# Kernel optimization log

Hardware: AMD Instinct MI355X
Metric: run time of the kernel (lower is better)

## Reference

```python
import jax, jax.numpy as jnp
import numpy as np

B, T, C, H = 8, 1024, 768, 12
M = 8  # extra rows in feats left as zeros (n = M + B*T)
N = M + B * T


def setup_inputs() -> dict:
    key = jax.random.key(0)
    k1, k2, k3, k4, k5 = jax.random.split(key, 5)
    feats = jax.random.normal(k1, (N, C), dtype=jnp.float32)
    amask = jax.random.randint(k2, (B, T), 0, 2).astype(bool)
    Wqkv = jax.random.normal(k3, (3 * C, C), dtype=jnp.float32) * 0.02
    Wp = jax.random.normal(k4, (C, C), dtype=jnp.float32) * 0.02
    bp = jax.random.normal(k5, (C,), dtype=jnp.float32) * 0.001
    return {"feats": feats, "amask": amask, "Wqkv": Wqkv, "Wp": Wp, "bp": bp}


def reference(feats, amask, Wqkv, Wp, bp):
    b, t = amask.shape
    n, c = feats.shape
    m = n - b * t          # rows of feats not touched by attention (stay zero)
    h = H
    d = c // h
    scale = d ** -0.5
    mf = amask.reshape(-1)                      # [b*t] bool
    x = feats[m:]                               # [b*t, c]

    # MaskedLinear(qkv): gather->GEMM->scatter == dense GEMM zeroed at masked-out rows
    qkv = jnp.where(mf[:, None], x @ Wqkv.T, jnp.zeros((), x.dtype))  # [b*t, 3c]
    qkv = qkv.reshape(b, t, 3, h, d).transpose(2, 0, 3, 1, 4)          # [3,b,h,t,d]
    q, k, v = qkv[0], qkv[1], qkv[2]

    # dense SDPA (no attn mask, matching F.scaled_dot_product_attention default)
    att = jax.nn.softmax(jnp.einsum('bhqd,bhkd->bhqk', q, k) * scale, axis=-1)
    o = jnp.einsum('bhqk,bhkd->bhqd', att, v)                          # [b,h,t,d]
    o = o.transpose(0, 2, 1, 3).reshape(b * t, c)                      # [b*t, c]

    # MaskedLinear(proj) with bias; masked-out rows are zero (not bias)
    o = jnp.where(mf[:, None], o @ Wp.T + bp, jnp.zeros((), o.dtype))

    # scatter back into a zero tensor of feats' shape (first m rows zero)
    return jnp.concatenate([jnp.zeros((m, c), feats.dtype), o], axis=0)
```

## Files before the change

### kernel.cpp

```cpp
#include <hip/hip_runtime.h>
#include <hip/hip_bf16.h>


#define BB 8
#define TT 1024
#define CC 768
#define HH 12
#define DD 64
#define MM 8
#define NTOK (BB*TT)
#define NX (NTOK*CC)
#define NWQ (3*CC*CC)
#define NWP (CC*CC)
#define QSCALE 0.18033688011112042f

typedef short bf16x4 __attribute__((ext_vector_type(4)));
typedef short bf16x8 __attribute__((ext_vector_type(8)));
typedef float f32x4  __attribute__((ext_vector_type(4)));
typedef float f32x16 __attribute__((ext_vector_type(16)));
typedef unsigned int u32x2 __attribute__((ext_vector_type(2)));

__device__ __forceinline__ void gld16(const void* g, void* l) {
  __builtin_amdgcn_global_load_lds(
      (const __attribute__((address_space(1))) void*)g,
      (__attribute__((address_space(3))) void*)l, 16, 0, 0);
}

__device__ __forceinline__ short bf_rne(float f) {
  unsigned u = __float_as_uint(f);
  return (short)((u + 0x7FFFu + ((u >> 16) & 1u)) >> 16);
}
__device__ __forceinline__ short bf_split(float f, short& lo) {
  unsigned u = __float_as_uint(f);
  unsigned hb = (u + 0x7FFFu + ((u >> 16) & 1u)) >> 16;
  float r = f - __uint_as_float(hb << 16);
  lo = bf_rne(r);
  return (short)hb;
}

__global__ __launch_bounds__(256) void split_inputs(
    const float* __restrict__ x, const float* __restrict__ wq,
    const float* __restrict__ wp,
    short* __restrict__ xh, short* __restrict__ wqh,
    short* __restrict__ wph, short* __restrict__ wpl,
    float* __restrict__ out) {
  const int G0 = NX/4, G1 = G0 + NWQ/4, G2 = G1 + NWP/4;
  int i = blockIdx.x * 256 + threadIdx.x;
  if (i < MM*CC/4) {
    float4 z = {0.f, 0.f, 0.f, 0.f};
    ((float4*)out)[i] = z;
  }
  if (i >= G2) return;
  if (i < G1) {
    const float* src = (i < G0) ? x : wq;
    short* dh = (i < G0) ? xh : wqh;
    int li = (i < G0) ? i : i - G0;
    float4 v = *(const float4*)(src + (size_t)li * 4);
    short4 h;
    h.x = bf_rne(v.x); h.y = bf_rne(v.y); h.z = bf_rne(v.z); h.w = bf_rne(v.w);
    *(short4*)(dh + (size_t)li * 4) = h;
  } else {
    int li = i - G1;
    float4 v = *(const float4*)(wp + (size_t)li * 4);
    short4 h, l;
    h.x = bf_split(v.x, l.x);
    h.y = bf_split(v.y, l.y);
    h.z = bf_split(v.z, l.z);
    h.w = bf_split(v.w, l.w);
    *(short4*)(wph + (size_t)li * 4) = h;
    *(short4*)(wpl + (size_t)li * 4) = l;
  }
}

template<bool TRIPLE>
__device__ __forceinline__ void gemm_core_768(
    const short* __restrict__ ah_g, const short* __restrict__ al_g,
    const short* __restrict__ bh_g, const short* __restrict__ bl_g,
    short* Ah, short* Al, short* Bh, short* Bl,
    int m0, int n0, f32x16 (&acc)[2][2],
    int& wm_o, int& wn_o) {
  const int tid = threadIdx.x;
  const int w = tid >> 6, ln = tid & 63;
  const int wm = (w >> 1) * 64, wn = (w & 1) * 64;
  const int sr = ln >> 2;
  const int sc = (((ln & 3) ^ ((ln >> 3) & 3))) * 8;
  const int l31 = ln & 31, lhi = ln >> 5;
  const int key = (l31 >> 1) & 3;
  const int c0 = 2*w, c1 = 2*w + 1;
  const short* gAh0 = ah_g + (size_t)(m0 + c0*16 + sr)*CC + sc;
  const short* gAh1 = ah_g + (size_t)(m0 + c1*16 + sr)*CC + sc;
  const short* gBh0 = bh_g + (size_t)(n0 + c0*16 + sr)*CC + sc;
  const short* gBh1 = bh_g + (size_t)(n0 + c1*16 + sr)*CC + sc;
  const short* gAl0 = TRIPLE ? al_g + (size_t)(m0 + c0*16 + sr)*CC + sc : nullptr;
  const short* gAl1 = TRIPLE ? al_g + (size_t)(m0 + c1*16 + sr)*CC + sc : nullptr;
  const short* gBl0 = TRIPLE ? bl_g + (size_t)(n0 + c0*16 + sr)*CC + sc : nullptr;
  const short* gBl1 = TRIPLE ? bl_g + (size_t)(n0 + c1*16 + sr)*CC + sc : nullptr;
  #pragma unroll
  for (int i = 0; i < 2; i++)
    #pragma unroll
    for (int j = 0; j < 2; j++)
      #pragma unroll
      for (int r = 0; r < 16; r++) acc[i][j][r] = 0.f;

  for (int it = 0; it < 24; ++it) {
    const int ko = it * 32;
    gld16(gAh0 + ko, &Ah[c0*512]);
    gld16(gAh1 + ko, &Ah[c1*512]);
    gld16(gBh0 + ko, &Bh[c0*512]);
    gld16(gBh1 + ko, &Bh[c1*512]);
    if constexpr (TRIPLE) {
      gld16(gAl0 + ko, &Al[c0*512]);
      gld16(gAl1 + ko, &Al[c1*512]);
      gld16(gBl0 + ko, &Bl[c0*512]);
      gld16(gBl1 + ko, &Bl[c1*512]);
    }
    __syncthreads();
    bf16x8 a_h[2][2], b_h[2][2];
    #pragma unroll
    for (int t = 0; t < 2; ++t)
      #pragma unroll
      for (int kc = 0; kc < 2; ++kc) {
        const int sA = ((kc*2 + lhi) ^ key) * 8;
        a_h[t][kc] = *(const bf16x8*)&Ah[(wm + t*32 + l31)*32 + sA];
        b_h[t][kc] = *(const bf16x8*)&Bh[(wn + t*32 + l31)*32 + sA];
      }
    if constexpr (TRIPLE) {
      bf16x8 a_l[2][2], b_l[2][2];
      #pragma unroll
      for (int t = 0; t < 2; ++t)
        #pragma unroll
        for (int kc = 0; kc < 2; ++kc) {
          const int sA = ((kc*2 + lhi) ^ key) * 8;
          a_l[t][kc] = *(const bf16x8*)&Al[(wm + t*32 + l31)*32 + sA];
          b_l[t][kc] = *(const bf16x8*)&Bl[(wn + t*32 + l31)*32 + sA];
        }
      #pragma unroll
      for (int mt = 0; mt < 2; ++mt)
        #pragma unroll
        for (int nt = 0; nt < 2; ++nt)
          #pragma unroll
          for (int kc = 0; kc < 2; ++kc) {
            acc[mt][nt] = __builtin_amdgcn_mfma_f32_32x32x16_bf16(
                a_h[mt][kc], b_h[nt][kc], acc[mt][nt], 0, 0, 0);
            acc[mt][nt] = __builtin_amdgcn_mfma_f32_32x32x16_bf16(
                a_h[mt][kc], b_l[nt][kc], acc[mt][nt], 0, 0, 0);
            acc[mt][nt] = __builtin_amdgcn_mfma_f32_32x32x16_bf16(
                a_l[mt][kc], b_h[nt][kc], acc[mt][nt], 0, 0, 0);
          }
    } else {
      #pragma unroll
      for (int mt = 0; mt < 2; ++mt)
        #pragma unroll
        for (int nt = 0; nt < 2; ++nt)
          #pragma unroll
          for (int kc = 0; kc < 2; ++kc)
            acc[mt][nt] = __builtin_amdgcn_mfma_f32_32x32x16_bf16(
                a_h[mt][kc], b_h[nt][kc], acc[mt][nt], 0, 0, 0);
    }
    __syncthreads();
  }
  wm_o = wm; wn_o = wn;
}

__global__ __launch_bounds__(256) void qkv_mfma(
    const short* __restrict__ xh, const short* __restrict__ wqh,
    const int* __restrict__ mask,
    short* __restrict__ qb, short* __restrict__ kb, short* __restrict__ vbt) {
  __shared__ __align__(16) short Ah[128*32], Bh[128*32];
  const int m0 = blockIdx.x * 128, n0 = blockIdx.y * 128;
  const int s = n0 / CC;
  f32x16 acc[2][2];
  int wm, wn;
  const int ln = threadIdx.x & 63;
  const int l31 = ln & 31, lhi = ln >> 5;

  if (s < 2) {
    gemm_core_768<false>(xh, nullptr, wqh, nullptr,
                         Ah, nullptr, Bh, nullptr, m0, n0, acc, wm, wn);
    short* dst = (s == 0) ? qb : kb;
    const float qs = (s == 0) ? QSCALE : 1.f;
    const int nb = n0 % CC;
    #pragma unroll
    for (int mt = 0; mt < 2; ++mt) {
      #pragma unroll
      for (int reg = 0; reg < 16; ++reg) {
        int row = m0 + wm + mt*32 + 4*lhi + (reg & 3) + 8*(reg >> 2);
        int mk = mask[row];
        int b = row >> 10, t = row & 1023;
        size_t rb = ((size_t)b * HH) * TT;
        #pragma unroll
        for (int nt = 0; nt < 2; ++nt) {
          int gnb = nb + wn + nt*32 + l31;
          int h = gnb >> 6, d = gnb & 63;
          float v = mk ? acc[mt][nt][reg] * qs : 0.f;
          dst[((rb + (size_t)h * TT) + t) * DD + d] = bf_rne(v);
        }
      }
    }
  } else {
    gemm_core_768<false>(wqh, nullptr, xh, nullptr,
                         Ah, nullptr, Bh, nullptr, n0, m0, acc, wm, wn);
    const int b = m0 >> 10, t0 = m0 & 1023;
    #pragma unroll
    for (int mt = 0; mt < 2; ++mt) {
      #pragma unroll
      for (int reg = 0; reg < 16; ++reg) {
        int f = (n0 - 2*CC) + wm + mt*32 + 4*lhi + (reg & 3) + 8*(reg >> 2);
        int h = f >> 6, d = f & 63;
        short* drow = vbt + (((size_t)(b*HH + h)*DD) + d)*TT + t0;
        #pragma unroll
        for (int nt = 0; nt < 2; ++nt) {
          int tk = wn + nt*32 + l31;
          int mk = mask[m0 + tk];
          drow[tk] = bf_rne(mk ? acc[mt][nt][reg] : 0.f);
        }
      }
    }
  }
}

__global__ __launch_bounds__(256) void proj_mfma(
    const short* __restrict__ ah_g, const short* __restrict__ al_g,
    const short* __restrict__ bh_g, const short* __restrict__ bl_g,
    const int* __restrict__ mask, const float* __restrict__ bp,
    float* __restrict__ out) {
  __shared__ __align__(16) short Ah[128*32], Al[128*32];
  __shared__ __align__(16) short Bh[128*32], Bl[128*32];
  const int m0 = blockIdx.x * 128, n0 = blockIdx.y * 128;
  f32x16 acc[2][2];
  int wm, wn;
  gemm_core_768<true>(ah_g, al_g, bh_g, bl_g, Ah, Al, Bh, Bl, m0, n0, acc, wm, wn);
  const int ln = threadIdx.x & 63;
  const int l31 = ln & 31, lhi = ln >> 5;
  #pragma unroll
  for (int mt = 0; mt < 2; ++mt) {
    #pragma unroll
    for (int reg = 0; reg < 16; ++reg) {
      int row = m0 + wm + mt*32 + 4*lhi + (reg & 3) + 8*(reg >> 2);
      int mk = mask[row];
      float* orow = out + (size_t)(MM + row) * CC;
      #pragma unroll
      for (int nt = 0; nt < 2; ++nt) {
        int gn = n0 + wn + nt*32 + l31;
        orow[gn] = mk ? acc[mt][nt][reg] + bp[gn] : 0.f;
      }
    }
  }
}

__device__ __forceinline__ bf16x4 tr64(unsigned addr, int imm) {
  bf16x4 r;
  asm volatile("ds_read_b64_tr_b16 %0, %1 offset:%c2"
               : "=v"(r) : "v"(addr), "i"(imm));
  return r;
}

__global__ __launch_bounds__(256, 3) void attn_mfma(
    const short* __restrict__ qb, const short* __restrict__ kb,
    const short* __restrict__ vbt, const int* __restrict__ mask,
    short* __restrict__ obh, short* __restrict__ obl) {
  __shared__ __align__(16) short Ks[64][72];
  __shared__ __align__(16) short Vt[64][72];
  __shared__ __align__(16) short PsT[4][2][64][16];
  const int tid = threadIdx.x, w = tid >> 6, ln = tid & 63;
  const int fl = ln & 15, fq = ln >> 4;
  const int i = blockIdx.x;
  const int bh = i % 96;
  const int q0 = (i / 96) * 128;
  const int b = bh / HH, h = bh % HH;
  const size_t baseK = (size_t)bh * TT * DD;
  const size_t baseV = (size_t)bh * DD * TT;

  bf16x8 qf[2][2];
  #pragma unroll
  for (int mt = 0; mt < 2; ++mt)
    #pragma unroll
    for (int kc = 0; kc < 2; ++kc)
      qf[mt][kc] = *(const bf16x8*)&qb[baseK +
          (size_t)(q0 + w*32 + mt*16 + fl) * DD + kc*32 + fq*8];

  f32x4 oa[2][4];
  float lsum[2][4];
  {
    f32x4 z = {0.f, 0.f, 0.f, 0.f};
    #pragma unroll
    for (int mt = 0; mt < 2; ++mt) {
      #pragma unroll
      for (int nt = 0; nt < 4; ++nt) oa[mt][nt] = z;
      #pragma unroll
      for (int r = 0; r < 4; ++r) lsum[mt][r] = 0.f;
    }
  }

  const unsigned ps_rd =
      (unsigned)(size_t)(&PsT[0][0][0][0]) + w*4096 + fq*256 + fl*8;

  const int srow = tid >> 2, scol = (tid & 3) * 16;
  const short* kg = &kb[baseK + (size_t)srow * DD + scol];
  const short* vg = &vbt[baseV + (size_t)srow * TT + scol];

  bf16x8 rk0 = *(const bf16x8*)kg;
  bf16x8 rk1 = *(const bf16x8*)(kg + 8);
  bf16x8 rv0 = *(const bf16x8*)vg;
  bf16x8 rv1 = *(const bf16x8*)(vg + 8);
  *(bf16x8*)&Ks[srow][scol]     = rk0;
  *(bf16x8*)&Ks[srow][scol + 8] = rk1;
  *(bf16x8*)&Vt[srow][scol]     = rv0;
  *(bf16x8*)&Vt[srow][scol + 8] = rv1;
  asm volatile("s_waitcnt lgkmcnt(0)" ::: "memory");
  __builtin_amdgcn_s_barrier();

  for (int kt = 0; kt < 16; ++kt) {
    if (kt < 15) {
      const short* kgn = kg + (size_t)(kt + 1) * 64 * DD;
      const short* vgn = vg + (kt + 1) * 64;
      rk0 = *(const bf16x8*)kgn;
      rk1 = *(const bf16x8*)(kgn + 8);
      rv0 = *(const bf16x8*)vgn;
      rv1 = *(const bf16x8*)(vgn + 8);
    }

    bf16x8 kf[4][2];
    #pragma unroll
    for (int nt = 0; nt < 4; ++nt)
      #pragma unroll
      for (int kc = 0; kc < 2; ++kc)
        kf[nt][kc] = *(const bf16x8*)&Ks[nt*16 + fl][kc*32 + fq*8];

    f32x4 s[2][4];
    {
      f32x4 z = {0.f, 0.f, 0.f, 0.f};
      #pragma unroll
      for (int mt = 0; mt < 2; ++mt)
        #pragma unroll
        for (int nt = 0; nt < 4; ++nt) s[mt][nt] = z;
    }
    #pragma unroll
    for (int mt = 0; mt < 2; ++mt)
      #pragma unroll
      for (int nt = 0; nt < 4; ++nt) {
        s[mt][nt] = __builtin_amdgcn_mfma_f32_16x16x32_bf16(
            qf[mt][0], kf[nt][0], s[mt][nt], 0, 0, 0);
        s[mt][nt] = __builtin_amdgcn_mfma_f32_16x16x32_bf16(
            qf[mt][1], kf[nt][1], s[mt][nt], 0, 0, 0);
      }

    bf16x8 vf[4][2];
    #pragma unroll
    for (int nt = 0; nt < 4; ++nt)
      #pragma unroll
      for (int kc = 0; kc < 2; ++kc)
        vf[nt][kc] = *(const bf16x8*)&Vt[nt*16 + fl][kc*32 + fq*8];

    #pragma unroll
    for (int mt = 0; mt < 2; ++mt)
      #pragma unroll
      for (int nt = 0; nt < 4; ++nt) {
        unsigned u0 = __float_as_uint(__builtin_amdgcn_exp2f(s[mt][nt][0]));
        unsigned u1 = __float_as_uint(__builtin_amdgcn_exp2f(s[mt][nt][1]));
        unsigned u2 = __float_as_uint(__builtin_amdgcn_exp2f(s[mt][nt][2]));
        unsigned u3 = __float_as_uint(__builtin_amdgcn_exp2f(s[mt][nt][3]));
        lsum[mt][0] += __uint_as_float(u0 & 0xFFFF0000u);
        lsum[mt][1] += __uint_as_float(u1 & 0xFFFF0000u);
        lsum[mt][2] += __uint_as_float(u2 & 0xFFFF0000u);
        lsum[mt][3] += __uint_as_float(u3 & 0xFFFF0000u);
        u32x2 pw;
        pw[0] = (u0 >> 16) | (u1 & 0xFFFF0000u);
        pw[1] = (u2 >> 16) | (u3 & 0xFFFF0000u);
        *(u32x2*)&PsT[w][mt][nt*16 + fl][fq*4] = pw;
      }

    asm volatile("s_waitcnt lgkmcnt(0)" ::: "memory");

    bf16x8 pf[2][2];
    #pragma unroll
    for (int mt = 0; mt < 2; ++mt)
      #pragma unroll
      for (int kc = 0; kc < 2; ++kc) {
        bf16x4 lo = tr64(ps_rd, mt*2048 + kc*1024);
        bf16x4 hi = tr64(ps_rd, mt*2048 + kc*1024 + 128);
        pf[mt][kc] = __builtin_shufflevector(lo, hi, 0, 1, 2, 3, 4, 5, 6, 7);
      }
    asm volatile("s_waitcnt lgkmcnt(0)" ::: "memory");
    __builtin_amdgcn_sched_barrier(0);

    #pragma unroll
    for (int mt = 0; mt < 2; ++mt)
      #pragma unroll
      for (int nt = 0; nt < 4; ++nt) {
        oa[mt][nt] = __builtin_amdgcn_mfma_f32_16x16x32_bf16(
            pf[mt][0], vf[nt][0], oa[mt][nt], 0, 0, 0);
        oa[mt][nt] = __builtin_amdgcn_mfma_f32_16x16x32_bf16(
            pf[mt][1], vf[nt][1], oa[mt][nt], 0, 0, 0);
      }

    __builtin_amdgcn_s_barrier();
    __builtin_amdgcn_sched_barrier(0);
    if (kt < 15) {
      *(bf16x8*)&Ks[srow][scol]     = rk0;
      *(bf16x8*)&Ks[srow][scol + 8] = rk1;
      *(bf16x8*)&Vt[srow][scol]     = rv0;
      *(bf16x8*)&Vt[srow][scol + 8] = rv1;
      asm volatile("s_waitcnt lgkmcnt(0)" ::: "memory");
    }
    __builtin_amdgcn_s_barrier();
  }

  #pragma unroll
  for (int mt = 0; mt < 2; ++mt)
    #pragma unroll
    for (int r = 0; r < 4; ++r) {
      float v = lsum[mt][r];
      v += __shfl_xor(v, 1);
      v += __shfl_xor(v, 2);
      v += __shfl_xor(v, 4);
      v += __shfl_xor(v, 8);
      lsum[mt][r] = v;
    }

  #pragma unroll
  for (int mt = 0; mt < 2; ++mt)
    #pragma unroll
    for (int r = 0; r < 4; ++r) {
      int tok = b * TT + q0 + w*32 + mt*16 + fq*4 + r;
      int mk = mask[tok];
      float inv = 1.f / lsum[mt][r];
      size_t ro = (size_t)tok * CC + h * DD;
      #pragma unroll
      for (int nt = 0; nt < 4; ++nt) {
        float v = mk ? oa[mt][nt][r] * inv : 0.f;
        short lo, hi = bf_split(v, lo);
        obh[ro + nt*16 + fl] = hi;
        obl[ro + nt*16 + fl] = lo;
      }
    }
}

extern "C" void kernel_launch(void* const* d_in, const int* in_sizes, int n_in,
                              void* d_out, int out_size, void* d_ws, size_t ws_size,
                              hipStream_t stream) {
  const float* feats = (const float*)d_in[0];
  const int*   mask  = (const int*)d_in[1];
  const float* Wqkv  = (const float*)d_in[2];
  const float* Wp    = (const float*)d_in[3];
  const float* bp    = (const float*)d_in[4];
  float* out = (float*)d_out;

  short* qb   = (short*)d_ws;
  short* kb   = qb + NX;
  short* vbt  = kb + NX;
  short* S_hi = vbt + NX;
  short* S_lo = S_hi + NX;
  short* wqh  = S_lo + NX;
  short* wph  = wqh + NWQ;
  short* wpl  = wph + NWP;

  const int G2 = (NX + NWQ + NWP) / 4;
  split_inputs<<<dim3((G2 + 255)/256), dim3(256), 0, stream>>>(
      feats + (size_t)MM * CC, Wqkv, Wp, S_hi, wqh, wph, wpl, out);
  qkv_mfma<<<dim3(NTOK/128, 3*CC/128), dim3(256), 0, stream>>>(
      S_hi, wqh, mask, qb, kb, vbt);
  attn_mfma<<<dim3(96 * (TT/128)), dim3(256), 0, stream>>>(
      qb, kb, vbt, mask, S_hi, S_lo);
  proj_mfma<<<dim3(NTOK/128, CC/128), dim3(256), 0, stream>>>(
      S_hi, S_lo, wph, wpl, mask, bp, out);
}
```

Measured before the change: 213.4 us.

## Double-buffer LDS tiles in GEMM core to overlap loads with MFMA

```diff
diff --git a/kernel.cpp b/kernel.cpp
--- a/kernel.cpp
+++ b/kernel.cpp
@@ -102,27 +102,30 @@
       #pragma unroll
       for (int r = 0; r < 16; r++) acc[i][j][r] = 0.f;
 
-  for (int it = 0; it < 24; ++it) {
-    const int ko = it * 32;
-    gld16(gAh0 + ko, &Ah[c0*512]);
-    gld16(gAh1 + ko, &Ah[c1*512]);
-    gld16(gBh0 + ko, &Bh[c0*512]);
-    gld16(gBh1 + ko, &Bh[c1*512]);
+  auto stage = [&](int hf, int it) {
+    const int ko = it * 32, off = hf * 4096;
+    gld16(gAh0 + ko, &Ah[off + c0*512]);
+    gld16(gAh1 + ko, &Ah[off + c1*512]);
+    gld16(gBh0 + ko, &Bh[off + c0*512]);
+    gld16(gBh1 + ko, &Bh[off + c1*512]);
     if constexpr (TRIPLE) {
-      gld16(gAl0 + ko, &Al[c0*512]);
-      gld16(gAl1 + ko, &Al[c1*512]);
-      gld16(gBl0 + ko, &Bl[c0*512]);
-      gld16(gBl1 + ko, &Bl[c1*512]);
-    }
-    __syncthreads();
+      gld16(gAl0 + ko, &Al[off + c0*512]);
+      gld16(gAl1 + ko, &Al[off + c1*512]);
+      gld16(gBl0 + ko, &Bl[off + c0*512]);
+      gld16(gBl1 + ko, &Bl[off + c1*512]);
+    }
+  };
+
+  auto compute = [&](int hf) {
+    const int off = hf * 4096;
     bf16x8 a_h[2][2], b_h[2][2];
     #pragma unroll
     for (int t = 0; t < 2; ++t)
       #pragma unroll
       for (int kc = 0; kc < 2; ++kc) {
         const int sA = ((kc*2 + lhi) ^ key) * 8;
-        a_h[t][kc] = *(const bf16x8*)&Ah[(wm + t*32 + l31)*32 + sA];
-        b_h[t][kc] = *(const bf16x8*)&Bh[(wn + t*32 + l31)*32 + sA];
+        a_h[t][kc] = *(const bf16x8*)&Ah[off + (wm + t*32 + l31)*32 + sA];
+        b_h[t][kc] = *(const bf16x8*)&Bh[off + (wn + t*32 + l31)*32 + sA];
       }
     if constexpr (TRIPLE) {
       bf16x8 a_l[2][2], b_l[2][2];
@@ -131,8 +134,8 @@
         #pragma unroll
         for (int kc = 0; kc < 2; ++kc) {
           const int sA = ((kc*2 + lhi) ^ key) * 8;
-          a_l[t][kc] = *(const bf16x8*)&Al[(wm + t*32 + l31)*32 + sA];
-          b_l[t][kc] = *(const bf16x8*)&Bl[(wn + t*32 + l31)*32 + sA];
+          a_l[t][kc] = *(const bf16x8*)&Al[off + (wm + t*32 + l31)*32 + sA];
+          b_l[t][kc] = *(const bf16x8*)&Bl[off + (wn + t*32 + l31)*32 + sA];
         }
       #pragma unroll
       for (int mt = 0; mt < 2; ++mt)
@@ -157,7 +160,25 @@
             acc[mt][nt] = __builtin_amdgcn_mfma_f32_32x32x16_bf16(
                 a_h[mt][kc], b_h[nt][kc], acc[mt][nt], 0, 0, 0);
     }
-    __syncthreads();
+  };
+
+  stage(0, 0);
+  asm volatile("s_waitcnt vmcnt(0)" ::: "memory");
+  __builtin_amdgcn_s_barrier();
+  __builtin_amdgcn_sched_barrier(0);
+
+  #pragma unroll 1
+  for (int it = 0; it < 24; it += 2) {
+    stage(1, it + 1);
+    compute(0);
+    asm volatile("s_waitcnt vmcnt(0)" ::: "memory");
+    __builtin_amdgcn_s_barrier();
+    __builtin_amdgcn_sched_barrier(0);
+    if (it + 2 < 24) stage(0, it + 2);
+    compute(1);
+    asm volatile("s_waitcnt vmcnt(0)" ::: "memory");
+    __builtin_amdgcn_s_barrier();
+    __builtin_amdgcn_sched_barrier(0);
   }
   wm_o = wm; wn_o = wn;
 }
@@ -166,7 +187,7 @@
     const short* __restrict__ xh, const short* __restrict__ wqh,
     const int* __restrict__ mask,
     short* __restrict__ qb, short* __restrict__ kb, short* __restrict__ vbt) {
-  __shared__ __align__(16) short Ah[128*32], Bh[128*32];
+  __shared__ __align__(16) short Ah[2*128*32], Bh[2*128*32];
   const int m0 = blockIdx.x * 128, n0 = blockIdx.y * 128;
   const int s = n0 / CC;
   f32x16 acc[2][2];
@@ -224,8 +245,8 @@
     const short* __restrict__ bh_g, const short* __restrict__ bl_g,
     const int* __restrict__ mask, const float* __restrict__ bp,
     float* __restrict__ out) {
-  __shared__ __align__(16) short Ah[128*32], Al[128*32];
-  __shared__ __align__(16) short Bh[128*32], Bl[128*32];
+  __shared__ __align__(16) short Ah[2*128*32], Al[2*128*32];
+  __shared__ __align__(16) short Bh[2*128*32], Bl[2*128*32];
   const int m0 = blockIdx.x * 128, n0 = blockIdx.y * 128;
   f32x16 acc[2][2];
   int wm, wn;
```

Result: slower. 230.3 us (+7.9%).

## Load QKV GEMM B operand directly to registers with double-buffered A tile

Applied to the files above, without the earlier changes.

```diff
diff --git a/kernel.cpp b/kernel.cpp
--- a/kernel.cpp
+++ b/kernel.cpp
@@ -72,8 +72,7 @@
   }
 }
 
-template<bool TRIPLE>
-__device__ __forceinline__ void gemm_core_768(
+__device__ __forceinline__ void gemm_core_triple(
     const short* __restrict__ ah_g, const short* __restrict__ al_g,
     const short* __restrict__ bh_g, const short* __restrict__ bl_g,
     short* Ah, short* Al, short* Bh, short* Bl,
@@ -91,10 +90,10 @@
   const short* gAh1 = ah_g + (size_t)(m0 + c1*16 + sr)*CC + sc;
   const short* gBh0 = bh_g + (size_t)(n0 + c0*16 + sr)*CC + sc;
   const short* gBh1 = bh_g + (size_t)(n0 + c1*16 + sr)*CC + sc;
-  const short* gAl0 = TRIPLE ? al_g + (size_t)(m0 + c0*16 + sr)*CC + sc : nullptr;
-  const short* gAl1 = TRIPLE ? al_g + (size_t)(m0 + c1*16 + sr)*CC + sc : nullptr;
-  const short* gBl0 = TRIPLE ? bl_g + (size_t)(n0 + c0*16 + sr)*CC + sc : nullptr;
-  const short* gBl1 = TRIPLE ? bl_g + (size_t)(n0 + c1*16 + sr)*CC + sc : nullptr;
+  const short* gAl0 = al_g + (size_t)(m0 + c0*16 + sr)*CC + sc;
+  const short* gAl1 = al_g + (size_t)(m0 + c1*16 + sr)*CC + sc;
+  const short* gBl0 = bl_g + (size_t)(n0 + c0*16 + sr)*CC + sc;
+  const short* gBl1 = bl_g + (size_t)(n0 + c1*16 + sr)*CC + sc;
   #pragma unroll
   for (int i = 0; i < 2; i++)
     #pragma unroll
@@ -108,14 +107,12 @@
     gld16(gAh1 + ko, &Ah[c1*512]);
     gld16(gBh0 + ko, &Bh[c0*512]);
     gld16(gBh1 + ko, &Bh[c1*512]);
-    if constexpr (TRIPLE) {
-      gld16(gAl0 + ko, &Al[c0*512]);
-      gld16(gAl1 + ko, &Al[c1*512]);
-      gld16(gBl0 + ko, &Bl[c0*512]);
-      gld16(gBl1 + ko, &Bl[c1*512]);
-    }
+    gld16(gAl0 + ko, &Al[c0*512]);
+    gld16(gAl1 + ko, &Al[c1*512]);
+    gld16(gBl0 + ko, &Bl[c0*512]);
+    gld16(gBl1 + ko, &Bl[c1*512]);
     __syncthreads();
-    bf16x8 a_h[2][2], b_h[2][2];
+    bf16x8 a_h[2][2], b_h[2][2], a_l[2][2], b_l[2][2];
     #pragma unroll
     for (int t = 0; t < 2; ++t)
       #pragma unroll
@@ -123,41 +120,101 @@
         const int sA = ((kc*2 + lhi) ^ key) * 8;
         a_h[t][kc] = *(const bf16x8*)&Ah[(wm + t*32 + l31)*32 + sA];
         b_h[t][kc] = *(const bf16x8*)&Bh[(wn + t*32 + l31)*32 + sA];
-      }
-    if constexpr (TRIPLE) {
-      bf16x8 a_l[2][2], b_l[2][2];
+        a_l[t][kc] = *(const bf16x8*)&Al[(wm + t*32 + l31)*32 + sA];
+        b_l[t][kc] = *(const bf16x8*)&Bl[(wn + t*32 + l31)*32 + sA];
+      }
+    #pragma unroll
+    for (int mt = 0; mt < 2; ++mt)
+      #pragma unroll
+      for (int nt = 0; nt < 2; ++nt)
+        #pragma unroll
+        for (int kc = 0; kc < 2; ++kc) {
+          acc[mt][nt] = __builtin_amdgcn_mfma_f32_32x32x16_bf16(
+              a_h[mt][kc], b_h[nt][kc], acc[mt][nt], 0, 0, 0);
+          acc[mt][nt] = __builtin_amdgcn_mfma_f32_32x32x16_bf16(
+              a_h[mt][kc], b_l[nt][kc], acc[mt][nt], 0, 0, 0);
+          acc[mt][nt] = __builtin_amdgcn_mfma_f32_32x32x16_bf16(
+              a_l[mt][kc], b_h[nt][kc], acc[mt][nt], 0, 0, 0);
+        }
+    __syncthreads();
+  }
+  wm_o = wm; wn_o = wn;
+}
+
+__device__ __forceinline__ void gemm_core_bdirect(
+    const short* __restrict__ a_g, const short* __restrict__ b_g,
+    short* Ah, int m0, int n0, f32x16 (&acc)[2][2],
+    int& wm_o, int& wn_o) {
+  const int tid = threadIdx.x;
+  const int w = tid >> 6, ln = tid & 63;
+  const int wm = (w >> 1) * 64, wn = (w & 1) * 64;
+  const int sr = ln >> 2;
+  const int sc = (((ln & 3) ^ ((ln >> 3) & 3))) * 8;
+  const int l31 = ln & 31, lhi = ln >> 5;
+  const int key = (l31 >> 1) & 3;
+  const int c0 = 2*w, c1 = 2*w + 1;
+  const short* gA0 = a_g + (size_t)(m0 + c0*16 + sr)*CC + sc;
+  const short* gA1 = a_g + (size_t)(m0 + c1*16 + sr)*CC + sc;
+  const short* gBb = b_g + (size_t)(n0 + wn + l31)*CC + lhi*8;
+  #pragma unroll
+  for (int i = 0; i < 2; i++)
+    #pragma unroll
+    for (int j = 0; j < 2; j++)
+      #pragma unroll
+      for (int r = 0; r < 16; r++) acc[i][j][r] = 0.f;
+
+  gld16(gA0, &Ah[c0*512]);
+  gld16(gA1, &Ah[c1*512]);
+  bf16x8 bc[2][2];
+  #pragma unroll
+  for (int t = 0; t < 2; ++t)
+    #pragma unroll
+    for (int kc = 0; kc < 2; ++kc)
+      bc[t][kc] = *(const bf16x8*)(gBb + (size_t)t*32*CC + kc*16);
+  asm volatile("s_waitcnt vmcnt(0)" ::: "memory");
+  __builtin_amdgcn_s_barrier();
+  __builtin_amdgcn_sched_barrier(0);
+
+  #pragma unroll 1
+  for (int it = 0; it < 24; ++it) {
+    const int hf = it & 1, nhf = hf ^ 1;
+    bf16x8 bn[2][2];
+    if (it < 23) {
+      const int ko = (it + 1) * 32;
+      gld16(gA0 + ko, &Ah[nhf*4096 + c0*512]);
+      gld16(gA1 + ko, &Ah[nhf*4096 + c1*512]);
       #pragma unroll
       for (int t = 0; t < 2; ++t)
         #pragma unroll
-        for (int kc = 0; kc < 2; ++kc) {
-          const int sA = ((kc*2 + lhi) ^ key) * 8;
-          a_l[t][kc] = *(const bf16x8*)&Al[(wm + t*32 + l31)*32 + sA];
-          b_l[t][kc] = *(const bf16x8*)&Bl[(wn + t*32 + l31)*32 + sA];
-        }
-      #pragma unroll
-      for (int mt = 0; mt < 2; ++mt)
-        #pragma unroll
-        for (int nt = 0; nt < 2; ++nt)
-          #pragma unroll
-          for (int kc = 0; kc < 2; ++kc) {
-            acc[mt][nt] = __builtin_amdgcn_mfma_f32_32x32x16_bf16(
-                a_h[mt][kc], b_h[nt][kc], acc[mt][nt], 0, 0, 0);
-            acc[mt][nt] = __builtin_amdgcn_mfma_f32_32x32x16_bf16(
-                a_h[mt][kc], b_l[nt][kc], acc[mt][nt], 0, 0, 0);
-            acc[mt][nt] = __builtin_amdgcn_mfma_f32_32x32x16_bf16(
-                a_l[mt][kc], b_h[nt][kc], acc[mt][nt], 0, 0, 0);
-          }
-    } else {
-      #pragma unroll
-      for (int mt = 0; mt < 2; ++mt)
-        #pragma unroll
-        for (int nt = 0; nt < 2; ++nt)
-          #pragma unroll
-          for (int kc = 0; kc < 2; ++kc)
-            acc[mt][nt] = __builtin_amdgcn_mfma_f32_32x32x16_bf16(
-                a_h[mt][kc], b_h[nt][kc], acc[mt][nt], 0, 0, 0);
-    }
-    __syncthreads();
+        for (int kc = 0; kc < 2; ++kc)
+          bn[t][kc] = *(const bf16x8*)(gBb + (size_t)t*32*CC + kc*16 + ko);
+    }
+    bf16x8 a_h[2][2];
+    #pragma unroll
+    for (int t = 0; t < 2; ++t)
+      #pragma unroll
+      for (int kc = 0; kc < 2; ++kc) {
+        const int sA = ((kc*2 + lhi) ^ key) * 8;
+        a_h[t][kc] = *(const bf16x8*)&Ah[hf*4096 + (wm + t*32 + l31)*32 + sA];
+      }
+    #pragma unroll
+    for (int mt = 0; mt < 2; ++mt)
+      #pragma unroll
+      for (int nt = 0; nt < 2; ++nt)
+        #pragma unroll
+        for (int kc = 0; kc < 2; ++kc)
+          acc[mt][nt] = __builtin_amdgcn_mfma_f32_32x32x16_bf16(
+              a_h[mt][kc], bc[nt][kc], acc[mt][nt], 0, 0, 0);
+    if (it < 23) {
+      #pragma unroll
+      for (int t = 0; t < 2; ++t)
+        #pragma unroll
+        for (int kc = 0; kc < 2; ++kc)
+          bc[t][kc] = bn[t][kc];
+    }
+    asm volatile("s_waitcnt vmcnt(0)" ::: "memory");
+    __builtin_amdgcn_s_barrier();
+    __builtin_amdgcn_sched_barrier(0);
   }
   wm_o = wm; wn_o = wn;
 }
@@ -166,7 +223,7 @@
     const short* __restrict__ xh, const short* __restrict__ wqh,
     const int* __restrict__ mask,
     short* __restrict__ qb, short* __restrict__ kb, short* __restrict__ vbt) {
-  __shared__ __align__(16) short Ah[128*32], Bh[128*32];
+  __shared__ __align__(16) short Ah[2*128*32];
   const int m0 = blockIdx.x * 128, n0 = blockIdx.y * 128;
   const int s = n0 / CC;
   f32x16 acc[2][2];
@@ -175,8 +232,7 @@
   const int l31 = ln & 31, lhi = ln >> 5;
 
   if (s < 2) {
-    gemm_core_768<false>(xh, nullptr, wqh, nullptr,
-                         Ah, nullptr, Bh, nullptr, m0, n0, acc, wm, wn);
+    gemm_core_bdirect(xh, wqh, Ah, m0, n0, acc, wm, wn);
     short* dst = (s == 0) ? qb : kb;
     const float qs = (s == 0) ? QSCALE : 1.f;
     const int nb = n0 % CC;
@@ -198,8 +254,7 @@
       }
     }
   } else {
-    gemm_core_768<false>(wqh, nullptr, xh, nullptr,
-                         Ah, nullptr, Bh, nullptr, n0, m0, acc, wm, wn);
+    gemm_core_bdirect(wqh, xh, Ah, n0, m0, acc, wm, wn);
     const int b = m0 >> 10, t0 = m0 & 1023;
     #pragma unroll
     for (int mt = 0; mt < 2; ++mt) {
@@ -229,7 +284,7 @@
   const int m0 = blockIdx.x * 128, n0 = blockIdx.y * 128;
   f32x16 acc[2][2];
   int wm, wn;
-  gemm_core_768<true>(ah_g, al_g, bh_g, bl_g, Ah, Al, Bh, Bl, m0, n0, acc, wm, wn);
+  gemm_core_triple(ah_g, al_g, bh_g, bl_g, Ah, Al, Bh, Bl, m0, n0, acc, wm, wn);
   const int ln = threadIdx.x & 63;
   const int l31 = ln & 31, lhi = ln >> 5;
   #pragma unroll
```

Result: slower. 251.3 us (+17.8%).

## Double-buffer K/V tiles in LDS via direct global-to-LDS loads with XOR swizzle

Applied to the files above, without the earlier changes.

```diff
diff --git a/kernel.cpp b/kernel.cpp
--- a/kernel.cpp
+++ b/kernel.cpp
@@ -259,8 +259,8 @@
     const short* __restrict__ qb, const short* __restrict__ kb,
     const short* __restrict__ vbt, const int* __restrict__ mask,
     short* __restrict__ obh, short* __restrict__ obl) {
-  __shared__ __align__(16) short Ks[64][72];
-  __shared__ __align__(16) short Vt[64][72];
+  __shared__ __align__(16) short Ks[2][64*64];
+  __shared__ __align__(16) short Vt[2][64*64];
   __shared__ __align__(16) short PsT[4][2][64][16];
   const int tid = threadIdx.x, w = tid >> 6, ln = tid & 63;
   const int fl = ln & 15, fq = ln >> 4;
@@ -295,37 +295,38 @@
   const unsigned ps_rd =
       (unsigned)(size_t)(&PsT[0][0][0][0]) + w*4096 + fq*256 + fl*8;
 
-  const int srow = tid >> 2, scol = (tid & 3) * 16;
-  const short* kg = &kb[baseK + (size_t)srow * DD + scol];
-  const short* vg = &vbt[baseV + (size_t)srow * TT + scol];
-
-  bf16x8 rk0 = *(const bf16x8*)kg;
-  bf16x8 rk1 = *(const bf16x8*)(kg + 8);
-  bf16x8 rv0 = *(const bf16x8*)vg;
-  bf16x8 rv1 = *(const bf16x8*)(vg + 8);
-  *(bf16x8*)&Ks[srow][scol]     = rk0;
-  *(bf16x8*)&Ks[srow][scol + 8] = rk1;
-  *(bf16x8*)&Vt[srow][scol]     = rv0;
-  *(bf16x8*)&Vt[srow][scol + 8] = rv1;
-  asm volatile("s_waitcnt lgkmcnt(0)" ::: "memory");
+  const int r1 = tid >> 3, r2 = r1 + 32;
+  const int g1 = ((ln & 7) ^ (r1 & 7)) * 8;
+  const int g2 = ((ln & 7) ^ (r2 & 7)) * 8;
+  const short* kg1 = &kb[baseK + (size_t)r1 * DD + g1];
+  const short* kg2 = &kb[baseK + (size_t)r2 * DD + g2];
+  const short* vg1 = &vbt[baseV + (size_t)r1 * TT + g1];
+  const short* vg2 = &vbt[baseV + (size_t)r2 * TT + g2];
+
+  auto stage = [&](int p, int kt) {
+    gld16(kg1 + (size_t)kt * 64 * DD, &Ks[p][w * 512]);
+    gld16(kg2 + (size_t)kt * 64 * DD, &Ks[p][2048 + w * 512]);
+    gld16(vg1 + kt * 64, &Vt[p][w * 512]);
+    gld16(vg2 + kt * 64, &Vt[p][2048 + w * 512]);
+  };
+
+  stage(0, 0);
+  asm volatile("s_waitcnt vmcnt(0)" ::: "memory");
   __builtin_amdgcn_s_barrier();
+  __builtin_amdgcn_sched_barrier(0);
 
   for (int kt = 0; kt < 16; ++kt) {
-    if (kt < 15) {
-      const short* kgn = kg + (size_t)(kt + 1) * 64 * DD;
-      const short* vgn = vg + (kt + 1) * 64;
-      rk0 = *(const bf16x8*)kgn;
-      rk1 = *(const bf16x8*)(kgn + 8);
-      rv0 = *(const bf16x8*)vgn;
-      rv1 = *(const bf16x8*)(vgn + 8);
-    }
+    const int p = kt & 1;
+    if (kt < 15) stage(p ^ 1, kt + 1);
 
     bf16x8 kf[4][2];
     #pragma unroll
     for (int nt = 0; nt < 4; ++nt)
       #pragma unroll
-      for (int kc = 0; kc < 2; ++kc)
-        kf[nt][kc] = *(const bf16x8*)&Ks[nt*16 + fl][kc*32 + fq*8];
+      for (int kc = 0; kc < 2; ++kc) {
+        const int sl = ((kc*4 + fq) ^ (fl & 7)) * 8;
+        kf[nt][kc] = *(const bf16x8*)&Ks[p][(nt*16 + fl)*64 + sl];
+      }
 
     f32x4 s[2][4];
     {
@@ -349,8 +350,10 @@
     #pragma unroll
     for (int nt = 0; nt < 4; ++nt)
       #pragma unroll
-      for (int kc = 0; kc < 2; ++kc)
-        vf[nt][kc] = *(const bf16x8*)&Vt[nt*16 + fl][kc*32 + fq*8];
+      for (int kc = 0; kc < 2; ++kc) {
+        const int sl = ((kc*4 + fq) ^ (fl & 7)) * 8;
+        vf[nt][kc] = *(const bf16x8*)&Vt[p][(nt*16 + fl)*64 + sl];
+      }
 
     #pragma unroll
     for (int mt = 0; mt < 2; ++mt)
@@ -394,16 +397,9 @@
             pf[mt][1], vf[nt][1], oa[mt][nt], 0, 0, 0);
       }
 
+    asm volatile("s_waitcnt vmcnt(0)" ::: "memory");
     __builtin_amdgcn_s_barrier();
     __builtin_amdgcn_sched_barrier(0);
-    if (kt < 15) {
-      *(bf16x8*)&Ks[srow][scol]     = rk0;
-      *(bf16x8*)&Ks[srow][scol + 8] = rk1;
-      *(bf16x8*)&Vt[srow][scol]     = rv0;
-      *(bf16x8*)&Vt[srow][scol + 8] = rv1;
-      asm volatile("s_waitcnt lgkmcnt(0)" ::: "memory");
-    }
-    __builtin_amdgcn_s_barrier();
   }
 
   #pragma unroll
```

New measurement: 214.7 us. About the same (+0.6%).
